# Performance work log

Hardware: AMD Instinct MI355X
Metric: run time of the kernel (lower is better)

## Reference

```python
import jax, jax.numpy as jnp
import numpy as np

B, T, C, L = 256, 256, 1024, 32
NEG = -1e30   # log-domain 'zero'
EPS = 1e-7    # keras.backend.epsilon()


def setup_inputs() -> dict:
    key = jax.random.key(0)
    k1, k2 = jax.random.split(key)
    # ctc_batch_cost expects softmax probabilities
    y_pred = jax.nn.softmax(jax.random.normal(k1, (B, T, C), dtype=jnp.float32), axis=-1)
    # labels in [1, C-2]: 0 is padding (count_nonzero), C-1 is the CTC blank
    y_true = jax.random.randint(k2, (B, L), 1, C - 1).astype(jnp.int32)
    return {"y_true": y_true, "y_pred": y_pred}


def _ctc_batch_cost(y_true, y_pred):
    b, t, c = y_pred.shape
    blank = c - 1                                   # TF ctc_loss: blank = last class
    lp = jnp.log(y_pred + EPS)                      # [B,T,C]
    l = y_true.shape[1]
    s = 2 * l + 1                                   # extended label length
    labels = y_true.astype(jnp.int32)
    # extended label seq: blank, l1, blank, l2, ..., blank
    ext = jnp.full((b, s), blank, jnp.int32).at[:, 1::2].set(labels)  # [B,S]
    label_len = jnp.sum((y_true != 0).astype(jnp.int32), axis=1)      # [B]
    # gather per-step log-probs of extended labels -> [B,T,S]
    lp_ext = jnp.take_along_axis(lp, jnp.broadcast_to(ext[:, None, :], (b, t, s)), axis=2)
    # skip transition s-2 -> s allowed iff ext[s] != blank and ext[s] != ext[s-2]
    prev2 = jnp.concatenate([jnp.full((b, 2), -1, jnp.int32), ext[:, :-2]], axis=1)
    allow_skip = (ext != blank) & (ext != prev2)    # [B,S]

    alpha = jnp.full((b, s), NEG, lp.dtype)
    alpha = alpha.at[:, 0].set(lp_ext[:, 0, 0]).at[:, 1].set(lp_ext[:, 0, 1])
    lp_t = jnp.transpose(lp_ext, (1, 0, 2))         # [T,B,S]

    def step(a, lpt):
        a1 = a
        a2 = jnp.concatenate([jnp.full((b, 1), NEG, a.dtype), a[:, :-1]], axis=1)
        a3 = jnp.concatenate([jnp.full((b, 2), NEG, a.dtype), a[:, :-2]], axis=1)
        a3 = jnp.where(allow_skip, a3, NEG)
        a_new = lpt + jnp.logaddexp(jnp.logaddexp(a1, a2), a3)
        return a_new, None

    alpha, _ = jax.lax.scan(step, alpha, lp_t[1:])  # input_length == T (full)
    bi = jnp.arange(b)
    idx_last_blank = 2 * label_len                  # position 2*Lb (last blank)
    idx_last_label = 2 * label_len - 1
    loss = -jnp.logaddexp(alpha[bi, idx_last_blank], alpha[bi, idx_last_label])
    return loss[:, None]                            # [B,1], matches ctc_batch_cost


def reference(y_true, y_pred):
    return _ctc_batch_cost(y_true, y_pred)
```

## Files before the change

kernel.cpp:

```cpp
#include <hip/hip_runtime.h>
#include <math.h>


#define Bt 256
#define Tt 256
#define Ct 1024
#define Lt 32
#define St 65
#define SP 66
#define CH 64
#define NCH (Tt / CH)
#define NEGV (-1e30f)
#define EPSV (1e-7f)

__device__ __forceinline__ float lae2(float a, float b) {
    float m = fmaxf(a, b);
    return m + __logf(__expf(a - m) + __expf(b - m));
}

__device__ __forceinline__ float lae3(float a, float b, float c) {
    float m = fmaxf(fmaxf(a, b), c);
    return m + __logf(__expf(a - m) + __expf(b - m) + __expf(c - m));
}

__global__ __launch_bounds__(256) void ctc_kernel(const int* __restrict__ y_true,
                                                  const float* __restrict__ y_pred,
                                                  float* __restrict__ out) {
    __shared__ float lp[2][CH][SP];
    __shared__ int ext_cls[St];
    __shared__ unsigned char skip_ok[St];
    __shared__ int s_ll;
    __shared__ float alpha_f[SP];

    const int b = blockIdx.x;
    const int tid = threadIdx.x;
    const int lane = tid & 63;
    const int blank = Ct - 1;
    const float* yp = y_pred + (size_t)b * Tt * Ct;
    const int* lab = y_true + b * Lt;

    if (tid < St) {
        int cls = blank;
        if (tid & 1) cls = lab[(tid - 1) >> 1];
        ext_cls[tid] = cls;
    }
    __syncthreads();
    if (tid < St) {
        int ok = 0;
        if (tid & 1) {
            int prev2 = (tid >= 2) ? ext_cls[tid - 2] : -1;
            ok = (ext_cls[tid] != blank && ext_cls[tid] != prev2) ? 1 : 0;
        }
        skip_ok[tid] = (unsigned char)ok;
    }
    if (tid == 0) {
        int ll = 0;
        for (int j = 0; j < Lt; ++j) ll += (lab[j] != 0) ? 1 : 0;
        s_ll = ll;
    }
    __syncthreads();

    for (int idx = tid; idx < CH * St; idx += 256) {
        int tt = idx / St;
        int s = idx - tt * St;
        lp[0][tt][s] = __logf(yp[tt * Ct + ext_cls[s]] + EPSV);
    }
    __syncthreads();

    float a_even = NEGV, a_odd = NEGV;

    for (int c = 0; c < NCH; ++c) {
        const int cur = c & 1;
        if (tid >= 64) {
            if (c + 1 < NCH) {
                const int nxt = cur ^ 1;
                const int base_t = (c + 1) * CH;
                for (int idx = tid - 64; idx < CH * St; idx += 192) {
                    int tt = idx / St;
                    int s = idx - tt * St;
                    lp[nxt][tt][s] = __logf(yp[(base_t + tt) * Ct + ext_cls[s]] + EPSV);
                }
            }
        } else {
            #pragma unroll 4
            for (int tt = 0; tt < CH; ++tt) {
                const bool act = (lane < 33);
                float le = NEGV, lo = NEGV;
                if (act) {
                    le = lp[cur][tt][2 * lane];
                    if (lane < 32) lo = lp[cur][tt][2 * lane + 1];
                }
                float pe = __shfl_up(a_even, 1);
                float po = __shfl_up(a_odd, 1);
                if (lane == 0) { pe = NEGV; po = NEGV; }
                (void)pe;
                if (act) {
                    int g = c * CH + tt;
                    if (g == 0) {
                        a_even = (lane == 0) ? le : NEGV;
                        a_odd  = (lane == 0) ? lo : NEGV;
                    } else {
                        float ne = le + lae2(a_even, po);
                        float no = NEGV;
                        if (lane < 32) {
                            float a3 = skip_ok[2 * lane + 1] ? po : NEGV;
                            no = lo + lae3(a_odd, a_even, a3);
                        }
                        a_even = ne;
                        a_odd = no;
                    }
                }
            }
        }
        __syncthreads();
    }

    if (tid < 64 && lane < 33) {
        alpha_f[2 * lane] = a_even;
        if (lane < 32) alpha_f[2 * lane + 1] = a_odd;
    }
    __syncthreads();
    if (tid == 0) {
        int ll = s_ll;
        int i1 = 2 * ll;
        int i2 = 2 * ll - 1;
        float v1 = alpha_f[i1];
        float v2 = (i2 >= 0) ? alpha_f[i2] : NEGV;
        out[b] = -lae2(v1, v2);
    }
}

extern "C" void kernel_launch(void* const* d_in, const int* in_sizes, int n_in,
                              void* d_out, int out_size, void* d_ws, size_t ws_size,
                              hipStream_t stream) {
    const int* y_true = (const int*)d_in[0];
    const float* y_pred = (const float*)d_in[1];
    float* out = (float*)d_out;
    (void)in_sizes; (void)n_in; (void)out_size; (void)d_ws; (void)ws_size;
    ctc_kernel<<<Bt, 256, 0, stream>>>(y_true, y_pred, out);
}
```

Baseline: 354.0 us.

## Preload all unique label log-probs with 16 waves, then run recursion barrier-free

```diff
diff --git a/kernel.cpp b/kernel.cpp
--- a/kernel.cpp
+++ b/kernel.cpp
@@ -6,127 +6,92 @@
 #define Tt 256
 #define Ct 1024
 #define Lt 32
-#define St 65
-#define SP 66
-#define CH 64
-#define NCH (Tt / CH)
 #define NEGV (-1e30f)
 #define EPSV (1e-7f)
+#define WAVES 16
+#define TPW (Tt / WAVES)
+#define STRIDE 33
 
 __device__ __forceinline__ float lae2(float a, float b) {
     float m = fmaxf(a, b);
     return m + __logf(__expf(a - m) + __expf(b - m));
 }
-
 __device__ __forceinline__ float lae3(float a, float b, float c) {
     float m = fmaxf(fmaxf(a, b), c);
     return m + __logf(__expf(a - m) + __expf(b - m) + __expf(c - m));
 }
 
-__global__ __launch_bounds__(256) void ctc_kernel(const int* __restrict__ y_true,
-                                                  const float* __restrict__ y_pred,
-                                                  float* __restrict__ out) {
-    __shared__ float lp[2][CH][SP];
-    __shared__ int ext_cls[St];
-    __shared__ unsigned char skip_ok[St];
-    __shared__ int s_ll;
-    __shared__ float alpha_f[SP];
+__global__ __launch_bounds__(1024) void ctc_kernel(const int* __restrict__ y_true,
+                                                   const float* __restrict__ y_pred,
+                                                   float* __restrict__ out) {
+    __shared__ float s_lp[Tt * STRIDE];
+    __shared__ float s_alpha[66];
 
     const int b = blockIdx.x;
     const int tid = threadIdx.x;
+    const int w = tid >> 6;
     const int lane = tid & 63;
     const int blank = Ct - 1;
     const float* yp = y_pred + (size_t)b * Tt * Ct;
     const int* lab = y_true + b * Lt;
 
-    if (tid < St) {
-        int cls = blank;
-        if (tid & 1) cls = lab[(tid - 1) >> 1];
-        ext_cls[tid] = cls;
-    }
-    __syncthreads();
-    if (tid < St) {
-        int ok = 0;
-        if (tid & 1) {
-            int prev2 = (tid >= 2) ? ext_cls[tid - 2] : -1;
-            ok = (ext_cls[tid] != blank && ext_cls[tid] != prev2) ? 1 : 0;
-        }
-        skip_ok[tid] = (unsigned char)ok;
-    }
-    if (tid == 0) {
-        int ll = 0;
-        for (int j = 0; j < Lt; ++j) ll += (lab[j] != 0) ? 1 : 0;
-        s_ll = ll;
+    int cls = blank;
+    if (lane < 32) cls = lab[lane];
+
+    if (lane < 33) {
+        const int t0 = w * TPW;
+        float v[TPW];
+        #pragma unroll
+        for (int k = 0; k < TPW; ++k)
+            v[k] = yp[(size_t)(t0 + k) * Ct + cls];
+        #pragma unroll
+        for (int k = 0; k < TPW; ++k)
+            s_lp[(t0 + k) * STRIDE + lane] = __logf(v[k] + EPSV);
     }
     __syncthreads();
 
-    for (int idx = tid; idx < CH * St; idx += 256) {
-        int tt = idx / St;
-        int s = idx - tt * St;
-        lp[0][tt][s] = __logf(yp[tt * Ct + ext_cls[s]] + EPSV);
-    }
-    __syncthreads();
+    if (w == 0) {
+        bool allow = true;
+        if (lane >= 1 && lane < 32) {
+            int lprev = lab[lane - 1];
+            allow = (cls != blank) && (cls != lprev);
+        }
 
-    float a_even = NEGV, a_odd = NEGV;
+        unsigned long long nz = __ballot(lane < 32 && cls != 0);
+        int ll = (int)__popcll(nz);
 
-    for (int c = 0; c < NCH; ++c) {
-        const int cur = c & 1;
-        if (tid >= 64) {
-            if (c + 1 < NCH) {
-                const int nxt = cur ^ 1;
-                const int base_t = (c + 1) * CH;
-                for (int idx = tid - 64; idx < CH * St; idx += 192) {
-                    int tt = idx / St;
-                    int s = idx - tt * St;
-                    lp[nxt][tt][s] = __logf(yp[(base_t + tt) * Ct + ext_cls[s]] + EPSV);
-                }
-            }
-        } else {
-            #pragma unroll 4
-            for (int tt = 0; tt < CH; ++tt) {
-                const bool act = (lane < 33);
-                float le = NEGV, lo = NEGV;
-                if (act) {
-                    le = lp[cur][tt][2 * lane];
-                    if (lane < 32) lo = lp[cur][tt][2 * lane + 1];
-                }
-                float pe = __shfl_up(a_even, 1);
-                float po = __shfl_up(a_odd, 1);
-                if (lane == 0) { pe = NEGV; po = NEGV; }
-                (void)pe;
-                if (act) {
-                    int g = c * CH + tt;
-                    if (g == 0) {
-                        a_even = (lane == 0) ? le : NEGV;
-                        a_odd  = (lane == 0) ? lo : NEGV;
-                    } else {
-                        float ne = le + lae2(a_even, po);
-                        float no = NEGV;
-                        if (lane < 32) {
-                            float a3 = skip_ok[2 * lane + 1] ? po : NEGV;
-                            no = lo + lae3(a_odd, a_even, a3);
-                        }
-                        a_even = ne;
-                        a_odd = no;
-                    }
-                }
-            }
+        float a_even, a_odd;
+        {
+            float le = s_lp[32];
+            float lo = (lane < 32) ? s_lp[lane] : NEGV;
+            a_even = (lane == 0) ? le : NEGV;
+            a_odd  = (lane == 0) ? lo : NEGV;
         }
-        __syncthreads();
-    }
 
-    if (tid < 64 && lane < 33) {
-        alpha_f[2 * lane] = a_even;
-        if (lane < 32) alpha_f[2 * lane + 1] = a_odd;
-    }
-    __syncthreads();
-    if (tid == 0) {
-        int ll = s_ll;
-        int i1 = 2 * ll;
-        int i2 = 2 * ll - 1;
-        float v1 = alpha_f[i1];
-        float v2 = (i2 >= 0) ? alpha_f[i2] : NEGV;
-        out[b] = -lae2(v1, v2);
+        #pragma unroll 4
+        for (int t = 1; t < Tt; ++t) {
+            float le = s_lp[t * STRIDE + 32];
+            float lo = (lane < 32) ? s_lp[t * STRIDE + lane] : NEGV;
+            float po = __shfl_up(a_odd, 1);
+            if (lane == 0) po = NEGV;
+            float ne = le + lae2(a_even, po);
+            float no = lo + lae3(a_odd, a_even, allow ? po : NEGV);
+            a_even = ne;
+            a_odd  = no;
+        }
+
+        if (lane < 33) {
+            s_alpha[2 * lane] = a_even;
+            if (lane < 32) s_alpha[2 * lane + 1] = a_odd;
+        }
+        __builtin_amdgcn_s_waitcnt(0);
+        if (lane == 0) {
+            int i1 = 2 * ll;
+            int i2 = 2 * ll - 1;
+            float v1 = s_alpha[i1];
+            float v2 = (i2 >= 0) ? s_alpha[i2] : NEGV;
+            out[b] = -lae2(v1, v2);
+        }
     }
 }
 
@@ -137,5 +102,5 @@
     const float* y_pred = (const float*)d_in[1];
     float* out = (float*)d_out;
     (void)in_sizes; (void)n_in; (void)out_size; (void)d_ws; (void)ws_size;
-    ctc_kernel<<<Bt, 256, 0, stream>>>(y_true, y_pred, out);
+    ctc_kernel<<<Bt, 1024, 0, stream>>>(y_true, y_pred, out);
 }
```

Result: slower. 375.4 us (+6.0%).
